# Performance work log

Hardware: AMD Instinct MI355X
Metric: run time of the kernel (lower is better)

Reference implementation:

```python
import jax, jax.numpy as jnp
import numpy as np

B, N, M, C, K = 2, 8192, 4096, 64, 16
HID = 256
EPS_BN = 1e-5


def setup_inputs() -> dict:
    key = jax.random.key(0)
    ks = jax.random.split(key, 16)
    def rn(i, shape, scale=1.0):
        return jax.random.normal(ks[i], shape, jnp.float32) * scale
    return {
        "pcl": rn(0, (B, M, 3)),
        "pcl_noise": rn(1, (B, N, 3)),
        "feature": rn(2, (B, M, C)),
        # MLP_CONV (2d 1x1): 6 -> 256 (BN+ReLU) -> C
        "w2a": rn(3, (HID, 6), 0.3), "b2a": rn(4, (HID,), 0.1),
        "g2a": 1.0 + rn(5, (HID,), 0.1), "bt2a": rn(6, (HID,), 0.1),
        "w2b": rn(7, (C, HID), 0.1), "b2b": rn(8, (C,), 0.1),
        # MLP_CONV_1d: 3C -> C (BN+ReLU) -> C
        "w1a": rn(9, (C, 3 * C), 0.1), "b1a": rn(10, (C,), 0.1),
        "g1a": 1.0 + rn(11, (C,), 0.1), "bt1a": rn(12, (C,), 0.1),
        "w1b": rn(13, (C, C), 0.1), "b1b": rn(14, (C,), 0.1),
    }


def _sqdist(x, y):  # [B,n,3],[B,m,3] -> [B,n,m]
    return (jnp.sum(x * x, -1, keepdims=True)
            - 2.0 * jnp.einsum('bnc,bmc->bnm', x, y)
            + jnp.sum(y * y, -1)[:, None, :])


def _gather(x, idx):  # x [B,M,D], idx [B,...] -> [B,...,D]
    return jax.vmap(lambda xb, ib: xb[ib])(x, idx)


def _bn(h, g, b):  # inference BatchNorm: running mean 0, var 1
    return h * (g / jnp.sqrt(1.0 + EPS_BN)) + b


def reference(pcl, pcl_noise, feature, w2a, b2a, g2a, bt2a, w2b, b2b,
              w1a, b1a, g1a, bt1a, w1b, b1b):
    # nearest clean point for each noisy point (knn_points K=1)
    close_idx = jnp.argmin(_sqdist(pcl_noise, pcl), axis=-1)          # [B,N]
    close_point = _gather(pcl, close_idx)                             # [B,N,3]
    # K nearest neighbors of close_point within pcl (dil_knn, d=1)
    _, idx = jax.lax.top_k(-_sqdist(close_point, pcl), K)             # [B,N,K]
    knn_points = _gather(pcl, idx)[:, :, 1:, :]                       # [B,N,K-1,3]
    knn_feat = _gather(feature, idx)[:, :, 1:, :]                     # [B,N,K-1,C]
    close_feat = _gather(feature, close_idx)                          # [B,N,C]

    delta = knn_points - pcl_noise[:, :, None, :]                     # [B,N,K-1,3]
    dst = jnp.linalg.norm(delta, axis=-1)                             # [B,N,K-1]
    e = jnp.exp(-10.0 * dst)
    weight = e / (jnp.sum(e, -1, keepdims=True) + 1e-7)               # [B,N,K-1]

    cp = jnp.broadcast_to(close_point[:, :, None, :], delta.shape)
    delta_points = jnp.concatenate([delta, cp], axis=-1)              # [B,N,K-1,6]

    # MLP_CONV2 (1x1 convs over channel dim)
    h = jnp.einsum('bnkc,oc->bnko', delta_points, w2a) + b2a
    h = jax.nn.relu(_bn(h, g2a, bt2a))
    pf = jnp.einsum('bnkc,oc->bnko', h, w2b) + b2b                    # [B,N,K-1,C]

    point_feature = jnp.einsum('bnk,bnkc->bnc', weight, pf)           # [B,N,C]
    co_feature = jnp.einsum('bnk,bnkc->bnc', weight, knn_feat)        # [B,N,C]
    df = jnp.concatenate([close_feat, co_feature, point_feature], -1)  # [B,N,3C]

    # MLP_CONV_1d
    h1 = jnp.einsum('bnc,oc->bno', df, w1a) + b1a
    h1 = jax.nn.relu(_bn(h1, g1a, bt1a))
    return jnp.einsum('bnc,oc->bno', h1, w1b) + b1b                   # [B,N,C]
```

## Files before the change

kernel.cpp:

```cpp
#include <hip/hip_runtime.h>
#include <float.h>

typedef unsigned short u16;
typedef unsigned int u32;
typedef unsigned char u8;

__device__ __forceinline__ float bf(u16 u) { return __uint_as_float(((u32)u) << 16); }
__device__ __forceinline__ u16 f2bf(float v) {
    u32 x = __float_as_uint(v);
    u32 r = x + 0x7fffu + ((x >> 16) & 1u);
    return (u16)(r >> 16);
}
__device__ __forceinline__ float blo(u32 u) { return __uint_as_float(u << 16); }
__device__ __forceinline__ float bhi(u32 u) { return __uint_as_float(u & 0xffff0000u); }
__device__ __forceinline__ int detect_f32(const void* probe) {
    const u16* u = (const u16*)probe;
    u16 v = u[(threadIdx.x & 63) * 2];
    int e = (int)((v >> 7) & 0xFF);
    int moderate = (e >= 100) && (e <= 140);
    return __popcll(__ballot(moderate)) < 48;
}
__device__ __forceinline__ float ldv(int f32, const void* p, int i) {
    return f32 ? ((const float*)p)[i] : bf(((const u16*)p)[i]);
}
__device__ __forceinline__ float dot3(float x0, float x1, float x2,
                                      float y0, float y1, float y2) {
    return __fmaf_rn(x2, y2, __fmaf_rn(x1, y1, __fmul_rn(x0, y0)));
}
__device__ __forceinline__ u32 mkey32(float d) {
    u32 f = __float_as_uint(d);
    return f ^ (u32)((((int)f) >> 31) | 0x80000000);
}

__global__ __launch_bounds__(256) void k_canon(const void* __restrict__ probe,
                                               const void* __restrict__ w2b,
                                               const void* __restrict__ w1a,
                                               const void* __restrict__ w1b,
                                               u32* __restrict__ canonb) {
    int f32 = detect_f32(probe);
    int ix = blockIdx.x * 256 + threadIdx.x;
    const void* src; int j;
    if (ix < 8192)       { src = w2b; j = ix; }
    else if (ix < 14336) { src = w1a; j = ix - 8192; }
    else                 { src = w1b; j = ix - 14336; }
    u32 out;
    if (f32) {
        const float* f = (const float*)src;
        out = ((u32)f2bf(f[2*j+1]) << 16) | (u32)f2bf(f[2*j]);
    } else {
        const u16* su = (const u16*)src;
        out = ((u32)su[2*j+1] << 16) | (u32)su[2*j];
    }
    canonb[ix] = out;
}

__global__ __launch_bounds__(256) void k_prep(const void* __restrict__ probe,
                                              const void* __restrict__ pcl,
                                              float4* __restrict__ pcl4) {
    int f32 = detect_f32(probe);
    int i = blockIdx.x * 256 + threadIdx.x;
    float x = ldv(f32, pcl, i*3+0), y = ldv(f32, pcl, i*3+1), z = ldv(f32, pcl, i*3+2);
    float s = __fadd_rn(__fadd_rn(__fmul_rn(x,x), __fmul_rn(y,y)), __fmul_rn(z,z));
    pcl4[i] = make_float4(x, y, z, s);
}

__global__ __launch_bounds__(256) void k_close(const float4* __restrict__ pcl4,
                                               const void* __restrict__ noise,
                                               u16* __restrict__ cidx) {
    __shared__ __align__(16) float4 tile[2048];
    int f32 = detect_f32(noise);
    int t = threadIdx.x, g = t >> 4, s = t & 15;
    int q = blockIdx.x * 16 + g;
    int b = q >> 13;
    const float4* src = pcl4 + ((size_t)b << 12);
    float x0 = ldv(f32, noise, q*3+0), x1 = ldv(f32, noise, q*3+1), x2 = ldv(f32, noise, q*3+2);
    float sx = __fadd_rn(__fadd_rn(__fmul_rn(x0,x0), __fmul_rn(x1,x1)), __fmul_rn(x2,x2));
    float bd = FLT_MAX; int bi = 0;
    for (int ch = 0; ch < 2; ++ch) {
        __syncthreads();
#pragma unroll
        for (int i = 0; i < 8; ++i) { int ix = t + (i << 8); tile[ix] = src[(ch << 11) + ix]; }
        __syncthreads();
        for (int j = 0; j < 128; ++j) {
            int cl = (j << 4) + s;
            float4 p = tile[cl];
            float dot = dot3(x0, x1, x2, p.x, p.y, p.z);
            float d = __fadd_rn(__fsub_rn(sx, __fmul_rn(2.0f, dot)), p.w);
            int c = (ch << 11) + cl;
            if (d < bd) { bd = d; bi = c; }
        }
    }
#pragma unroll
    for (int m = 8; m >= 1; m >>= 1) {
        float od = __shfl_xor(bd, m);
        int   oi = __shfl_xor(bi, m);
        if (od < bd || (od == bd && oi < bi)) { bd = od; bi = oi; }
    }
    if (s == 0) cidx[q] = (u16)(bi & 4095);
}

__global__ __launch_bounds__(256) void k_knnh(const float4* __restrict__ pcl4,
                                              u16* __restrict__ knn) {
    __shared__ u8  bins[4096];
    __shared__ u32 hist[256];
    __shared__ u32 skey[256];
    __shared__ u16 sidx[256];
    __shared__ float rmn[4], rmx[4];
    __shared__ u32 scnt;
    __shared__ int ibst;
    int t = threadIdx.x, lane = t & 63, wv = t >> 6;
    int q = blockIdx.x;
    int b = q >> 12;
    const float4* src = pcl4 + ((size_t)b << 12);
    float4 Q = src[q & 4095];
    float x0 = Q.x, x1 = Q.y, x2 = Q.z, sx = Q.w;
    if (t < 256) hist[t] = 0;
    if (t == 0) scnt = 0;
    {
        float4 p = src[t << 4];
        float dot = dot3(x0, x1, x2, p.x, p.y, p.z);
        float d = __fadd_rn(__fsub_rn(sx, __fmul_rn(2.0f, dot)), p.w);
        float mn = d, mx = d;
#pragma unroll
        for (int m = 32; m >= 1; m >>= 1) {
            mn = fminf(mn, __shfl_xor(mn, m));
            mx = fmaxf(mx, __shfl_xor(mx, m));
        }
        if (lane == 0) { rmn[wv] = mn; rmx[wv] = mx; }
    }
    __syncthreads();
    float dmn = fminf(fminf(rmn[0], rmn[1]), fminf(rmn[2], rmn[3]));
    float dmx = fmaxf(fmaxf(rmx[0], rmx[1]), fmaxf(rmx[2], rmx[3]));
    float sc = 1024.0f / fmaxf(dmx - dmn, 1e-20f);
#pragma unroll 4
    for (int j = 0; j < 16; ++j) {
        int cin = (j << 8) + t;
        float4 p = src[cin];
        float dot = dot3(x0, x1, x2, p.x, p.y, p.z);
        float d = __fadd_rn(__fsub_rn(sx, __fmul_rn(2.0f, dot)), p.w);
        float fb = fminf(fmaxf((d - dmn) * sc, 0.0f), 255.0f);
        int bn = (int)fb;
        bins[cin] = (u8)bn;
        if (bn < 255) atomicAdd(&hist[bn], 1u);
    }
    __syncthreads();
    if (t < 64) {
        u32 c0 = hist[4*lane], c1 = hist[4*lane+1];
        u32 c2 = hist[4*lane+2], c3 = hist[4*lane+3];
        u32 loc = c0 + c1 + c2 + c3;
        u32 x = loc;
#pragma unroll
        for (int off = 1; off < 64; off <<= 1) { u32 v = __shfl_up(x, off); if (lane >= off) x += v; }
        u32 excl = x - loc;
        int cand = 999;
        if (excl + c0 >= 16u) cand = 4*lane;
        else if (excl + c0 + c1 >= 16u) cand = 4*lane + 1;
        else if (excl + c0 + c1 + c2 >= 16u) cand = 4*lane + 2;
        else if (excl + loc >= 16u) cand = 4*lane + 3;
#pragma unroll
        for (int m = 32; m >= 1; m >>= 1) cand = min(cand, __shfl_xor(cand, m));
        if (lane == 0) ibst = cand;
    }
    __syncthreads();
    int bstar = ibst;
#pragma unroll
    for (int j = 0; j < 16; ++j) {
        int cin = (j << 8) + t;
        if ((int)bins[cin] <= bstar) {
            u32 pos = atomicAdd(&scnt, 1u);
            if (pos < 256u) {
                float4 p = src[cin];
                float dot = dot3(x0, x1, x2, p.x, p.y, p.z);
                float d = __fadd_rn(__fsub_rn(sx, __fmul_rn(2.0f, dot)), p.w);
                skey[pos] = mkey32(d);
                sidx[pos] = (u16)cin;
            }
        }
    }
    __syncthreads();
    u32 n = scnt;
    if (n <= 256u) {
        for (u32 e = (u32)t; e < n; e += 256u) {
            u32 k = skey[e]; u32 i = (u32)sidx[e];
            int rank = 0;
            for (u32 j = 0; j < n; ++j) {
                u32 kj = skey[j]; u32 ij = (u32)sidx[j];
                rank += (kj < k) || (kj == k && ij < i);
            }
            if (rank < 16) knn[((size_t)q << 4) + rank] = (u16)i;
        }
    } else if (t < 64) {
        u32 k0=~0u,k1=~0u,k2=~0u,k3=~0u,k4=~0u,k5=~0u,k6=~0u,k7=~0u,
            k8=~0u,k9=~0u,k10=~0u,k11=~0u,k12=~0u,k13=~0u,k14=~0u,k15=~0u;
        u32 i0r=0,i1r=0,i2r=0,i3r=0,i4r=0,i5r=0,i6r=0,i7r=0,
            i8r=0,i9r=0,i10r=0,i11r=0,i12r=0,i13r=0,i14r=0,i15r=0;
        for (int j = 0; j < 64; ++j) {
            int cin = (j << 6) + lane;
            float4 p = src[cin];
            float dot = dot3(x0, x1, x2, p.x, p.y, p.z);
            float d = __fadd_rn(__fsub_rn(sx, __fmul_rn(2.0f, dot)), p.w);
            u32 v = mkey32(d); u32 vi = (u32)cin;
            if (v < k15) {
                { u32 c_=(v<k0); u32 nk=c_?v:k0; u32 nv=c_?k0:v; u32 ni=c_?vi:i0r; u32 nj=c_?i0r:vi; k0=nk;i0r=ni;v=nv;vi=nj; }
                { u32 c_=(v<k1); u32 nk=c_?v:k1; u32 nv=c_?k1:v; u32 ni=c_?vi:i1r; u32 nj=c_?i1r:vi; k1=nk;i1r=ni;v=nv;vi=nj; }
                { u32 c_=(v<k2); u32 nk=c_?v:k2; u32 nv=c_?k2:v; u32 ni=c_?vi:i2r; u32 nj=c_?i2r:vi; k2=nk;i2r=ni;v=nv;vi=nj; }
                { u32 c_=(v<k3); u32 nk=c_?v:k3; u32 nv=c_?k3:v; u32 ni=c_?vi:i3r; u32 nj=c_?i3r:vi; k3=nk;i3r=ni;v=nv;vi=nj; }
                { u32 c_=(v<k4); u32 nk=c_?v:k4; u32 nv=c_?k4:v; u32 ni=c_?vi:i4r; u32 nj=c_?i4r:vi; k4=nk;i4r=ni;v=nv;vi=nj; }
                { u32 c_=(v<k5); u32 nk=c_?v:k5; u32 nv=c_?k5:v; u32 ni=c_?vi:i5r; u32 nj=c_?i5r:vi; k5=nk;i5r=ni;v=nv;vi=nj; }
                { u32 c_=(v<k6); u32 nk=c_?v:k6; u32 nv=c_?k6:v; u32 ni=c_?vi:i6r; u32 nj=c_?i6r:vi; k6=nk;i6r=ni;v=nv;vi=nj; }
                { u32 c_=(v<k7); u32 nk=c_?v:k7; u32 nv=c_?k7:v; u32 ni=c_?vi:i7r; u32 nj=c_?i7r:vi; k7=nk;i7r=ni;v=nv;vi=nj; }
                { u32 c_=(v<k8); u32 nk=c_?v:k8; u32 nv=c_?k8:v; u32 ni=c_?vi:i8r; u32 nj=c_?i8r:vi; k8=nk;i8r=ni;v=nv;vi=nj; }
                { u32 c_=(v<k9); u32 nk=c_?v:k9; u32 nv=c_?k9:v; u32 ni=c_?vi:i9r; u32 nj=c_?i9r:vi; k9=nk;i9r=ni;v=nv;vi=nj; }
                { u32 c_=(v<k10); u32 nk=c_?v:k10; u32 nv=c_?k10:v; u32 ni=c_?vi:i10r; u32 nj=c_?i10r:vi; k10=nk;i10r=ni;v=nv;vi=nj; }
                { u32 c_=(v<k11); u32 nk=c_?v:k11; u32 nv=c_?k11:v; u32 ni=c_?vi:i11r; u32 nj=c_?i11r:vi; k11=nk;i11r=ni;v=nv;vi=nj; }
                { u32 c_=(v<k12); u32 nk=c_?v:k12; u32 nv=c_?k12:v; u32 ni=c_?vi:i12r; u32 nj=c_?i12r:vi; k12=nk;i12r=ni;v=nv;vi=nj; }
                { u32 c_=(v<k13); u32 nk=c_?v:k13; u32 nv=c_?k13:v; u32 ni=c_?vi:i13r; u32 nj=c_?i13r:vi; k13=nk;i13r=ni;v=nv;vi=nj; }
                { u32 c_=(v<k14); u32 nk=c_?v:k14; u32 nv=c_?k14:v; u32 ni=c_?vi:i14r; u32 nj=c_?i14r:vi; k14=nk;i14r=ni;v=nv;vi=nj; }
                { u32 c_=(v<k15); u32 nk=c_?v:k15; u32 nv=c_?k15:v; u32 ni=c_?vi:i15r; u32 nj=c_?i15r:vi; k15=nk;i15r=ni;v=nv;vi=nj; }
            }
        }
        u32 myres = 0;
        for (int o = 0; o < 16; ++o) {
            u32 bk = k0, bi2 = i0r;
#pragma unroll
            for (int m = 32; m >= 1; m >>= 1) {
                u32 ok = __shfl_xor(bk, m), oi = __shfl_xor(bi2, m);
                if (ok < bk || (ok == bk && oi < bi2)) { bk = ok; bi2 = oi; }
            }
            if (lane == o) myres = bi2;
            if (k0 == bk && i0r == bi2) {
                k0=k1; i0r=i1r; k1=k2; i1r=i2r; k2=k3; i2r=i3r; k3=k4; i3r=i4r;
                k4=k5; i4r=i5r; k5=k6; i5r=i6r; k6=k7; i6r=i7r; k7=k8; i7r=i8r;
                k8=k9; i8r=i9r; k9=k10; i9r=i10r; k10=k11; i10r=i11r; k11=k12; i11r=i12r;
                k12=k13; i12r=i13r; k13=k14; i13r=i14r; k14=k15; i14r=i15r;
                k15=~0u; i15r=0xFFFFu;
            }
        }
        if (lane < 16) knn[((size_t)q << 4) + lane] = (u16)myres;
    }
}

__global__ __launch_bounds__(256) void k_tail(const float4* __restrict__ pcl4,
                                              const void* __restrict__ noise,
                                              const void* __restrict__ feat,
                                              const u16* __restrict__ cidx,
                                              const u16* __restrict__ knn,
                                              const void* __restrict__ w2a,
                                              const void* __restrict__ b2a,
                                              const void* __restrict__ g2a,
                                              const void* __restrict__ bt2a,
                                              const u32* __restrict__ canonb,
                                              const void* __restrict__ b2b,
                                              const void* __restrict__ b1a,
                                              const void* __restrict__ g1a,
                                              const void* __restrict__ bt1a,
                                              const void* __restrict__ b1b,
                                              void* __restrict__ outp) {
    __shared__ float w2at[6][256];
    __shared__ float sc2[256], of2[256];
    __shared__ float b2bf[64], s1[64], o1[64], b1f[64];
    __shared__ __align__(16) float hb[4][4][256];
    __shared__ __align__(16) float dfs[4][4][192];
    __shared__ __align__(16) float h1s[4][4][64];
    __shared__ float dpb[4][4][16][6];
    __shared__ float wbuf[4][4][16];
    __shared__ int   jbuf[4][4][16];
    __shared__ float wsb[4][4];

    int f32 = detect_f32(noise);
    int t = threadIdx.x;
    {
        float s2 = ldv(f32, g2a, t) / sqrtf(1.0f + 1e-5f);
        sc2[t] = s2;
        of2[t] = ldv(f32, b2a, t) * s2 + ldv(f32, bt2a, t);
#pragma unroll
        for (int c = 0; c < 6; ++c) w2at[c][t] = ldv(f32, w2a, t*6+c);
        if (t < 64) {
            b2bf[t] = ldv(f32, b2b, t);
            float s = ldv(f32, g1a, t) / sqrtf(1.0f + 1e-5f);
            s1[t] = s; o1[t] = ldv(f32, b1a, t) * s + ldv(f32, bt1a, t); b1f[t] = ldv(f32, b1b, t);
        }
    }
    int lane = t & 63, wv = t >> 6;
    int qbase = blockIdx.x * 16 + wv * 4;
    {
        int ql = lane >> 4, s = lane & 15;
        int q = qbase + ql;
        int b = q >> 13;
        int pbase = (b << 12);
        int ci = ((int)cidx[q]) & 4095;
        float4 cp = pcl4[pbase + ci];
        float x0 = ldv(f32, noise, q*3+0), x1 = ldv(f32, noise, q*3+1), x2 = ldv(f32, noise, q*3+2);
        float e = 0.0f;
        if (s >= 1) {
            int jk = ((int)knn[(size_t)(pbase + ci) * 16 + s]) & 4095;
            float4 p = pcl4[pbase + jk];
            float d0 = p.x - x0, d1 = p.y - x1, d2 = p.z - x2;
            float dst = sqrtf(__fadd_rn(__fadd_rn(__fmul_rn(d0,d0), __fmul_rn(d1,d1)), __fmul_rn(d2,d2)));
            e = expf(-10.0f * dst);
            dpb[wv][ql][s][0] = d0; dpb[wv][ql][s][1] = d1; dpb[wv][ql][s][2] = d2;
            dpb[wv][ql][s][3] = cp.x; dpb[wv][ql][s][4] = cp.y; dpb[wv][ql][s][5] = cp.z;
            jbuf[wv][ql][s] = jk;
        }
        float es = e;
#pragma unroll
        for (int m = 8; m >= 1; m >>= 1) es += __shfl_xor(es, m, 16);
        float den = es + 1e-7f;
        if (s >= 1) wbuf[wv][ql][s] = e / den;
        if (s == 0) wsb[wv][ql] = es / den;
    }
    __syncthreads();

    float cf[4], co[4];
#pragma unroll
    for (int ql = 0; ql < 4; ++ql) {
        int q = qbase + ql;
        int b = q >> 13;
        int pbase = (b << 12);
        int ci = ((int)cidx[q]) & 4095;
        size_t fcb = ((size_t)(pbase + ci)) << 6;
        float c0, c1 = 0.0f;
        if (f32) {
            const float* ff = (const float*)feat;
            c0 = ff[fcb + lane];
#pragma unroll
            for (int k = 1; k < 16; ++k)
                c1 += wbuf[wv][ql][k] * ff[(((size_t)(pbase + jbuf[wv][ql][k])) << 6) + lane];
        } else {
            const u16* fb = (const u16*)feat;
            c0 = bf(fb[fcb + lane]);
#pragma unroll
            for (int k = 1; k < 16; ++k)
                c1 += wbuf[wv][ql][k] * bf(fb[(((size_t)(pbase + jbuf[wv][ql][k])) << 6) + lane]);
        }
        cf[ql] = c0; co[ql] = c1;
    }

    float wa[4][6], scr[4], ofr[4];
#pragma unroll
    for (int r = 0; r < 4; ++r) {
        int ch = lane + (r << 6);
#pragma unroll
        for (int c = 0; c < 6; ++c) wa[r][c] = w2at[c][ch];
        scr[r] = sc2[ch]; ofr[r] = of2[ch];
    }
    float hv[4][4];
#pragma unroll
    for (int ql = 0; ql < 4; ++ql)
#pragma unroll
        for (int r = 0; r < 4; ++r) hv[ql][r] = 0.0f;
#pragma unroll
    for (int k = 1; k < 16; ++k) {
#pragma unroll
        for (int ql = 0; ql < 4; ++ql) {
            float p0 = dpb[wv][ql][k][0], p1 = dpb[wv][ql][k][1], p2 = dpb[wv][ql][k][2];
            float p3 = dpb[wv][ql][k][3], p4 = dpb[wv][ql][k][4], p5 = dpb[wv][ql][k][5];
            float wk = wbuf[wv][ql][k];
#pragma unroll
            for (int r = 0; r < 4; ++r) {
                float z = p0*wa[r][0] + p1*wa[r][1] + p2*wa[r][2]
                        + p3*wa[r][3] + p4*wa[r][4] + p5*wa[r][5];
                z = z * scr[r] + ofr[r];
                z = fmaxf(z, 0.0f);
                hv[ql][r] += wk * z;
            }
        }
    }
#pragma unroll
    for (int ql = 0; ql < 4; ++ql)
#pragma unroll
        for (int r = 0; r < 4; ++r) hb[wv][ql][lane + (r << 6)] = hv[ql][r];
    __syncthreads();

    float acc[4];
#pragma unroll
    for (int ql = 0; ql < 4; ++ql) acc[ql] = b2bf[lane] * wsb[wv][ql];
    {
        const uint4* wrow = reinterpret_cast<const uint4*>(canonb + (lane << 7));
#pragma unroll 4
        for (int i = 0; i < 32; ++i) {
            uint4 u = wrow[i];
            float w0 = blo(u.x), w1 = bhi(u.x), w2 = blo(u.y), w3 = bhi(u.y);
            float w4 = blo(u.z), w5 = bhi(u.z), w6 = blo(u.w), w7 = bhi(u.w);
#pragma unroll
            for (int ql = 0; ql < 4; ++ql) {
                const float4* hrow = reinterpret_cast<const float4*>(&hb[wv][ql][0]);
                float4 hA = hrow[2*i], hB = hrow[2*i+1];
                acc[ql] += w0*hA.x + w1*hA.y + w2*hA.z + w3*hA.w
                         + w4*hB.x + w5*hB.y + w6*hB.z + w7*hB.w;
            }
        }
    }
#pragma unroll
    for (int ql = 0; ql < 4; ++ql) {
        dfs[wv][ql][lane]       = cf[ql];
        dfs[wv][ql][64 + lane]  = co[ql];
        dfs[wv][ql][128 + lane] = acc[ql];
    }
    __syncthreads();

    float acc1[4] = {0.0f, 0.0f, 0.0f, 0.0f};
    {
        const uint4* wr = reinterpret_cast<const uint4*>(canonb + 8192 + lane * 96);
#pragma unroll 4
        for (int i = 0; i < 24; ++i) {
            uint4 u = wr[i];
            float w0 = blo(u.x), w1 = bhi(u.x), w2 = blo(u.y), w3 = bhi(u.y);
            float w4 = blo(u.z), w5 = bhi(u.z), w6 = blo(u.w), w7 = bhi(u.w);
#pragma unroll
            for (int ql = 0; ql < 4; ++ql) {
                const float4* dv = reinterpret_cast<const float4*>(&dfs[wv][ql][0]);
                float4 a = dv[2*i], c = dv[2*i+1];
                acc1[ql] += w0*a.x + w1*a.y + w2*a.z + w3*a.w
                          + w4*c.x + w5*c.y + w6*c.z + w7*c.w;
            }
        }
    }
#pragma unroll
    for (int ql = 0; ql < 4; ++ql) {
        float z1 = acc1[ql] * s1[lane] + o1[lane];
        z1 = fmaxf(z1, 0.0f);
        h1s[wv][ql][lane] = z1;
    }
    __syncthreads();

    float a2[4];
#pragma unroll
    for (int ql = 0; ql < 4; ++ql) a2[ql] = b1f[lane];
    {
        const uint4* wr2 = reinterpret_cast<const uint4*>(canonb + 14336 + (lane << 5));
#pragma unroll
        for (int i = 0; i < 8; ++i) {
            uint4 u = wr2[i];
            float w0 = blo(u.x), w1 = bhi(u.x), w2 = blo(u.y), w3 = bhi(u.y);
            float w4 = blo(u.z), w5 = bhi(u.z), w6 = blo(u.w), w7 = bhi(u.w);
#pragma unroll
            for (int ql = 0; ql < 4; ++ql) {
                const float4* hv2 = reinterpret_cast<const float4*>(&h1s[wv][ql][0]);
                float4 a = hv2[2*i], c = hv2[2*i+1];
                a2[ql] += w0*a.x + w1*a.y + w2*a.z + w3*a.w
                        + w4*c.x + w5*c.y + w6*c.z + w7*c.w;
            }
        }
    }
#pragma unroll
    for (int ql = 0; ql < 4; ++ql) {
        size_t ob = ((size_t)(qbase + ql) << 6) + lane;
        if (f32) ((float*)outp)[ob] = a2[ql];
        else     ((u16*)outp)[ob]   = f2bf(a2[ql]);
    }
}

extern "C" void kernel_launch(void* const* d_in, const int* in_sizes, int n_in,
                              void* d_out, int out_size, void* d_ws, size_t ws_size,
                              hipStream_t stream) {
    const void* pcl   = d_in[0];
    const void* noise = d_in[1];
    const void* feat  = d_in[2];
    const void* w2a   = d_in[3];
    const void* b2a   = d_in[4];
    const void* g2a   = d_in[5];
    const void* bt2a  = d_in[6];
    const void* w2b   = d_in[7];
    const void* b2b   = d_in[8];
    const void* w1a   = d_in[9];
    const void* b1a   = d_in[10];
    const void* g1a   = d_in[11];
    const void* bt1a  = d_in[12];
    const void* w1b   = d_in[13];
    const void* b1b   = d_in[14];

    char* ws = (char*)d_ws;
    float4* pcl4 = (float4*)ws;
    u16* cidx = (u16*)(ws + 131072);
    u16* knn  = (u16*)(ws + 163840);
    u32* canonb = (u32*)(ws + 425984);

    k_canon<<<64,   256, 0, stream>>>(noise, w2b, w1a, w1b, canonb);
    k_prep <<<32,   256, 0, stream>>>(noise, pcl, pcl4);
    k_close<<<1024, 256, 0, stream>>>(pcl4, noise, cidx);
    k_knnh <<<8192, 256, 0, stream>>>(pcl4, knn);
    k_tail <<<1024, 256, 0, stream>>>(pcl4, noise, feat, cidx, knn,
                                      w2a, b2a, g2a, bt2a, canonb, b2b,
                                      b1a, g1a, bt1a, b1b, d_out);
}
```

Baseline: 239.1 us.

## Move tail MLP layers onto bf16 MFMA with hi/lo split-precision operands

Rewrites the per-query MLP tail kernel so that the 6->256 conv, the 256->64 conv, and the two 1d layers run on 16x16x32 bf16 MFMA instructions instead of scalar FMA loops. Activations are split into bf16 high and low parts and accumulated with two MFMAs to keep near-fp32 accuracy. The first layer also folds the BN scale into the weights and uses a third operand slot for the low part of the weights. Shared memory is repacked into a single arena holding bf16 tiles, and a launch-bounds occupancy hint is added. This adds bf16 conversion overhead and some accuracy risk in exchange for much higher matrix throughput.

```diff
diff --git a/kernel.cpp b/kernel.cpp
--- a/kernel.cpp
+++ b/kernel.cpp
@@ -4,6 +4,9 @@
 typedef unsigned short u16;
 typedef unsigned int u32;
 typedef unsigned char u8;
+
+typedef float f32x4 __attribute__((ext_vector_type(4)));
+typedef short bh8   __attribute__((ext_vector_type(8)));
 
 __device__ __forceinline__ float bf(u16 u) { return __uint_as_float(((u32)u) << 16); }
 __device__ __forceinline__ u16 f2bf(float v) {
@@ -11,8 +14,6 @@
     u32 r = x + 0x7fffu + ((x >> 16) & 1u);
     return (u16)(r >> 16);
 }
-__device__ __forceinline__ float blo(u32 u) { return __uint_as_float(u << 16); }
-__device__ __forceinline__ float bhi(u32 u) { return __uint_as_float(u & 0xffff0000u); }
 __device__ __forceinline__ int detect_f32(const void* probe) {
     const u16* u = (const u16*)probe;
     u16 v = u[(threadIdx.x & 63) * 2];
@@ -30,6 +31,10 @@
 __device__ __forceinline__ u32 mkey32(float d) {
     u32 f = __float_as_uint(d);
     return f ^ (u32)((((int)f) >> 31) | 0x80000000);
+}
+__device__ __forceinline__ bh8 ldb(const void* p) { return *(const bh8*)p; }
+__device__ __forceinline__ f32x4 mfma16(bh8 a, bh8 b, f32x4 c) {
+    return __builtin_amdgcn_mfma_f32_16x16x32_bf16(a, b, c, 0, 0, 0);
 }
 
 __global__ __launch_bounds__(256) void k_canon(const void* __restrict__ probe,
@@ -240,54 +245,71 @@
     }
 }
 
-__global__ __launch_bounds__(256) void k_tail(const float4* __restrict__ pcl4,
-                                              const void* __restrict__ noise,
-                                              const void* __restrict__ feat,
-                                              const u16* __restrict__ cidx,
-                                              const u16* __restrict__ knn,
-                                              const void* __restrict__ w2a,
-                                              const void* __restrict__ b2a,
-                                              const void* __restrict__ g2a,
-                                              const void* __restrict__ bt2a,
-                                              const u32* __restrict__ canonb,
-                                              const void* __restrict__ b2b,
-                                              const void* __restrict__ b1a,
-                                              const void* __restrict__ g1a,
-                                              const void* __restrict__ bt1a,
-                                              const void* __restrict__ b1b,
-                                              void* __restrict__ outp) {
-    __shared__ float w2at[6][256];
-    __shared__ float sc2[256], of2[256];
-    __shared__ float b2bf[64], s1[64], o1[64], b1f[64];
-    __shared__ __align__(16) float hb[4][4][256];
-    __shared__ __align__(16) float dfs[4][4][192];
-    __shared__ __align__(16) float h1s[4][4][64];
-    __shared__ float dpb[4][4][16][6];
-    __shared__ float wbuf[4][4][16];
-    __shared__ int   jbuf[4][4][16];
-    __shared__ float wsb[4][4];
+__global__ __launch_bounds__(256, 4) void k_tail(const float4* __restrict__ pcl4,
+                                                 const void* __restrict__ noise,
+                                                 const void* __restrict__ feat,
+                                                 const u16* __restrict__ cidx,
+                                                 const u16* __restrict__ knn,
+                                                 const void* __restrict__ w2a,
+                                                 const void* __restrict__ b2a,
+                                                 const void* __restrict__ g2a,
+                                                 const void* __restrict__ bt2a,
+                                                 const u32* __restrict__ canonb,
+                                                 const void* __restrict__ b2b,
+                                                 const void* __restrict__ b1a,
+                                                 const void* __restrict__ g1a,
+                                                 const void* __restrict__ bt1a,
+                                                 const void* __restrict__ b1b,
+                                                 void* __restrict__ outp) {
+    __shared__ __align__(16) char arena[39744];
+    char* dpb_hi = arena;
+    char* dpb_lo = arena + 4352;
+    char* wbt    = arena + 8704;
+    char* wsbp   = arena + 9984;
+    u16*  jbuf   = (u16*)(arena + 10048);
+    char* hbm_   = arena + 10560;
+    char* dfm    = arena + 27200;
+    char* h1m    = arena;
 
     int f32 = detect_f32(noise);
-    int t = threadIdx.x;
+    int t = threadIdx.x, lane = t & 63, wv = t >> 6;
+    int g = lane >> 4, l15 = lane & 15;
+    int qbb = blockIdx.x * 16;
+    int o_lane = wv * 16 + l15;
+    const float rbn = 1.0f / sqrtf(1.0f + 1e-5f);
+    const char* cb = (const char*)canonb;
+    const f32x4 zero4 = {0.f, 0.f, 0.f, 0.f};
+
+    float of2r[4];
+    bh8 wH[4];
+#pragma unroll
+    for (int j = 0; j < 4; ++j) {
+        int oh = wv*64 + j*16 + l15;
+        float sc = ldv(f32, g2a, oh) * rbn;
+        of2r[j] = ldv(f32, b2a, oh) * sc + ldv(f32, bt2a, oh);
+        bh8 wz = (bh8){0,0,0,0,0,0,0,0};
+        if (g < 3) {
+#pragma unroll
+            for (int c = 0; c < 6; ++c) {
+                float wval = ldv(f32, w2a, oh*6 + c) * sc;
+                u16 h = f2bf(wval);
+                u16 e = (g == 2) ? f2bf(wval - bf(h)) : h;
+                wz[c] = (short)e;
+            }
+        }
+        wH[j] = wz;
+    }
+    float s1o  = ldv(f32, g1a, o_lane) * rbn;
+    float o1o  = ldv(f32, b1a, o_lane) * s1o + ldv(f32, bt1a, o_lane);
+    float b2bo = ldv(f32, b2b, o_lane);
+    float b1fo = ldv(f32, b1b, o_lane);
+
     {
-        float s2 = ldv(f32, g2a, t) / sqrtf(1.0f + 1e-5f);
-        sc2[t] = s2;
-        of2[t] = ldv(f32, b2a, t) * s2 + ldv(f32, bt2a, t);
-#pragma unroll
-        for (int c = 0; c < 6; ++c) w2at[c][t] = ldv(f32, w2a, t*6+c);
-        if (t < 64) {
-            b2bf[t] = ldv(f32, b2b, t);
-            float s = ldv(f32, g1a, t) / sqrtf(1.0f + 1e-5f);
-            s1[t] = s; o1[t] = ldv(f32, b1a, t) * s + ldv(f32, bt1a, t); b1f[t] = ldv(f32, b1b, t);
-        }
-    }
-    int lane = t & 63, wv = t >> 6;
-    int qbase = blockIdx.x * 16 + wv * 4;
-    {
-        int ql = lane >> 4, s = lane & 15;
-        int q = qbase + ql;
+        int s = lane & 15;
+        int ql = wv*4 + (lane >> 4);
+        int q = qbb + ql;
         int b = q >> 13;
-        int pbase = (b << 12);
+        int pbase = b << 12;
         int ci = ((int)cidx[q]) & 4095;
         float4 cp = pcl4[pbase + ci];
         float x0 = ldv(f32, noise, q*3+0), x1 = ldv(f32, noise, q*3+1), x2 = ldv(f32, noise, q*3+2);
@@ -298,25 +320,35 @@
             float d0 = p.x - x0, d1 = p.y - x1, d2 = p.z - x2;
             float dst = sqrtf(__fadd_rn(__fadd_rn(__fmul_rn(d0,d0), __fmul_rn(d1,d1)), __fmul_rn(d2,d2)));
             e = expf(-10.0f * dst);
-            dpb[wv][ql][s][0] = d0; dpb[wv][ql][s][1] = d1; dpb[wv][ql][s][2] = d2;
-            dpb[wv][ql][s][3] = cp.x; dpb[wv][ql][s][4] = cp.y; dpb[wv][ql][s][5] = cp.z;
-            jbuf[wv][ql][s] = jk;
+            float v6[6] = {d0, d1, d2, cp.x, cp.y, cp.z};
+            bh8 HW = (bh8){0,0,0,0,0,0,0,0};
+            bh8 LW = (bh8){0,0,0,0,0,0,0,0};
+#pragma unroll
+            for (int c = 0; c < 6; ++c) {
+                u16 hh = f2bf(v6[c]);
+                u16 ll = f2bf(v6[c] - bf(hh));
+                HW[c] = (short)hh;
+                LW[c] = (short)ll;
+            }
+            *(bh8*)(dpb_hi + (ql*17 + s)*16) = HW;
+            *(bh8*)(dpb_lo + (ql*17 + s)*16) = LW;
+            jbuf[ql*16 + s] = (u16)jk;
         }
         float es = e;
 #pragma unroll
         for (int m = 8; m >= 1; m >>= 1) es += __shfl_xor(es, m, 16);
         float den = es + 1e-7f;
-        if (s >= 1) wbuf[wv][ql][s] = e / den;
-        if (s == 0) wsb[wv][ql] = es / den;
-    }
-    __syncthreads();
-
-    float cf[4], co[4];
-#pragma unroll
-    for (int ql = 0; ql < 4; ++ql) {
-        int q = qbase + ql;
+        if (s >= 1) *(float*)(wbt + s*80 + ql*4) = e / den;
+        if (s == 0) *(float*)(wsbp + ql*4) = es / den;
+    }
+    __syncthreads();
+
+#pragma unroll
+    for (int qq = 0; qq < 4; ++qq) {
+        int qloc = wv*4 + qq;
+        int q = qbb + qloc;
         int b = q >> 13;
-        int pbase = (b << 12);
+        int pbase = b << 12;
         int ci = ((int)cidx[q]) & 4095;
         size_t fcb = ((size_t)(pbase + ci)) << 6;
         float c0, c1 = 0.0f;
@@ -324,130 +356,136 @@
             const float* ff = (const float*)feat;
             c0 = ff[fcb + lane];
 #pragma unroll
-            for (int k = 1; k < 16; ++k)
-                c1 += wbuf[wv][ql][k] * ff[(((size_t)(pbase + jbuf[wv][ql][k])) << 6) + lane];
+            for (int k = 1; k < 16; ++k) {
+                float wk = *(const float*)(wbt + k*80 + qloc*4);
+                c1 += wk * ff[(((size_t)(pbase + (int)jbuf[qloc*16 + k])) << 6) + lane];
+            }
         } else {
             const u16* fb = (const u16*)feat;
             c0 = bf(fb[fcb + lane]);
 #pragma unroll
-            for (int k = 1; k < 16; ++k)
-                c1 += wbuf[wv][ql][k] * bf(fb[(((size_t)(pbase + jbuf[wv][ql][k])) << 6) + lane]);
-        }
-        cf[ql] = c0; co[ql] = c1;
-    }
-
-    float wa[4][6], scr[4], ofr[4];
-#pragma unroll
-    for (int r = 0; r < 4; ++r) {
-        int ch = lane + (r << 6);
-#pragma unroll
-        for (int c = 0; c < 6; ++c) wa[r][c] = w2at[c][ch];
-        scr[r] = sc2[ch]; ofr[r] = of2[ch];
-    }
-    float hv[4][4];
-#pragma unroll
-    for (int ql = 0; ql < 4; ++ql)
-#pragma unroll
-        for (int r = 0; r < 4; ++r) hv[ql][r] = 0.0f;
-#pragma unroll
-    for (int k = 1; k < 16; ++k) {
-#pragma unroll
-        for (int ql = 0; ql < 4; ++ql) {
-            float p0 = dpb[wv][ql][k][0], p1 = dpb[wv][ql][k][1], p2 = dpb[wv][ql][k][2];
-            float p3 = dpb[wv][ql][k][3], p4 = dpb[wv][ql][k][4], p5 = dpb[wv][ql][k][5];
-            float wk = wbuf[wv][ql][k];
+            for (int k = 1; k < 16; ++k) {
+                float wk = *(const float*)(wbt + k*80 + qloc*4);
+                c1 += wk * bf(fb[(((size_t)(pbase + (int)jbuf[qloc*16 + k])) << 6) + lane]);
+            }
+        }
+        char* dr = dfm + qloc*784;
+        u16 h0 = f2bf(c0); u16 l0 = f2bf(c0 - bf(h0));
+        u16 h1v = f2bf(c1); u16 l1v = f2bf(c1 - bf(h1v));
+        *(u16*)(dr + (size_t)lane*2)         = h0;
+        *(u16*)(dr + (size_t)(192+lane)*2)   = l0;
+        *(u16*)(dr + (size_t)(64+lane)*2)    = h1v;
+        *(u16*)(dr + (size_t)(256+lane)*2)   = l1v;
+    }
+
+    {
+        f32x4 hba[4];
+#pragma unroll
+        for (int j = 0; j < 4; ++j) hba[j] = zero4;
+#pragma unroll
+        for (int k = 1; k < 16; ++k) {
+            bh8 af;
+            if (g < 3) {
+                const char* base = (g == 1) ? dpb_lo : dpb_hi;
+                af = ldb(base + (l15*17 + k)*16);
+            } else {
+                af = (bh8){0,0,0,0,0,0,0,0};
+            }
+            f32x4 wk4 = *(const f32x4*)(wbt + k*80 + g*16);
+#pragma unroll
+            for (int j = 0; j < 4; ++j) {
+                f32x4 d = mfma16(af, wH[j], zero4);
+#pragma unroll
+                for (int r = 0; r < 4; ++r)
+                    hba[j][r] += wk4[r] * fmaxf(d[r] + of2r[j], 0.0f);
+            }
+        }
+#pragma unroll
+        for (int j = 0; j < 4; ++j)
 #pragma unroll
             for (int r = 0; r < 4; ++r) {
-                float z = p0*wa[r][0] + p1*wa[r][1] + p2*wa[r][2]
-                        + p3*wa[r][3] + p4*wa[r][4] + p5*wa[r][5];
-                z = z * scr[r] + ofr[r];
-                z = fmaxf(z, 0.0f);
-                hv[ql][r] += wk * z;
-            }
-        }
-    }
-#pragma unroll
-    for (int ql = 0; ql < 4; ++ql)
-#pragma unroll
-        for (int r = 0; r < 4; ++r) hb[wv][ql][lane + (r << 6)] = hv[ql][r];
-    __syncthreads();
-
-    float acc[4];
-#pragma unroll
-    for (int ql = 0; ql < 4; ++ql) acc[ql] = b2bf[lane] * wsb[wv][ql];
+                int q = g*4 + r;
+                int o = wv*64 + j*16 + l15;
+                float x = hba[j][r];
+                u16 h = f2bf(x); u16 l = f2bf(x - bf(h));
+                *(u16*)(hbm_ + q*1040 + (size_t)o*2)       = h;
+                *(u16*)(hbm_ + q*1040 + 512 + (size_t)o*2) = l;
+            }
+    }
+    __syncthreads();
+
     {
-        const uint4* wrow = reinterpret_cast<const uint4*>(canonb + (lane << 7));
-#pragma unroll 4
-        for (int i = 0; i < 32; ++i) {
-            uint4 u = wrow[i];
-            float w0 = blo(u.x), w1 = bhi(u.x), w2 = blo(u.y), w3 = bhi(u.y);
-            float w4 = blo(u.z), w5 = bhi(u.z), w6 = blo(u.w), w7 = bhi(u.w);
-#pragma unroll
-            for (int ql = 0; ql < 4; ++ql) {
-                const float4* hrow = reinterpret_cast<const float4*>(&hb[wv][ql][0]);
-                float4 hA = hrow[2*i], hB = hrow[2*i+1];
-                acc[ql] += w0*hA.x + w1*hA.y + w2*hA.z + w3*hA.w
-                         + w4*hB.x + w5*hB.y + w6*hB.z + w7*hB.w;
-            }
-        }
-    }
-#pragma unroll
-    for (int ql = 0; ql < 4; ++ql) {
-        dfs[wv][ql][lane]       = cf[ql];
-        dfs[wv][ql][64 + lane]  = co[ql];
-        dfs[wv][ql][128 + lane] = acc[ql];
-    }
-    __syncthreads();
-
-    float acc1[4] = {0.0f, 0.0f, 0.0f, 0.0f};
+        bh8 bw[8];
+#pragma unroll
+        for (int ks = 0; ks < 8; ++ks)
+            bw[ks] = ldb(cb + (size_t)o_lane*512 + ks*64 + g*16);
+        f32x4 acA = zero4, acB = zero4;
+#pragma unroll
+        for (int ks = 0; ks < 8; ++ks) {
+            bh8 a = ldb(hbm_ + l15*1040 + ks*64 + g*16);
+            acA = mfma16(a, bw[ks], acA);
+        }
+#pragma unroll
+        for (int ks = 0; ks < 8; ++ks) {
+            bh8 a = ldb(hbm_ + l15*1040 + 512 + ks*64 + g*16);
+            acB = mfma16(a, bw[ks], acB);
+        }
+        f32x4 wsb4 = *(const f32x4*)(wsbp + g*16);
+#pragma unroll
+        for (int r = 0; r < 4; ++r) {
+            int q = g*4 + r;
+            float pf = acA[r] + acB[r] + b2bo * wsb4[r];
+            u16 h = f2bf(pf); u16 l = f2bf(pf - bf(h));
+            *(u16*)(dfm + q*784 + (size_t)(128 + o_lane)*2) = h;
+            *(u16*)(dfm + q*784 + (size_t)(320 + o_lane)*2) = l;
+        }
+    }
+    __syncthreads();
+
     {
-        const uint4* wr = reinterpret_cast<const uint4*>(canonb + 8192 + lane * 96);
-#pragma unroll 4
-        for (int i = 0; i < 24; ++i) {
-            uint4 u = wr[i];
-            float w0 = blo(u.x), w1 = bhi(u.x), w2 = blo(u.y), w3 = bhi(u.y);
-            float w4 = blo(u.z), w5 = bhi(u.z), w6 = blo(u.w), w7 = bhi(u.w);
-#pragma unroll
-            for (int ql = 0; ql < 4; ++ql) {
-                const float4* dv = reinterpret_cast<const float4*>(&dfs[wv][ql][0]);
-                float4 a = dv[2*i], c = dv[2*i+1];
-                acc1[ql] += w0*a.x + w1*a.y + w2*a.z + w3*a.w
-                          + w4*c.x + w5*c.y + w6*c.z + w7*c.w;
-            }
-        }
-    }
-#pragma unroll
-    for (int ql = 0; ql < 4; ++ql) {
-        float z1 = acc1[ql] * s1[lane] + o1[lane];
-        z1 = fmaxf(z1, 0.0f);
-        h1s[wv][ql][lane] = z1;
-    }
-    __syncthreads();
-
-    float a2[4];
-#pragma unroll
-    for (int ql = 0; ql < 4; ++ql) a2[ql] = b1f[lane];
+        bh8 bw[6];
+#pragma unroll
+        for (int ks = 0; ks < 6; ++ks)
+            bw[ks] = ldb(cb + 32768 + (size_t)o_lane*384 + ks*64 + g*16);
+        f32x4 acA = zero4, acB = zero4;
+#pragma unroll
+        for (int ks = 0; ks < 6; ++ks) {
+            bh8 a = ldb(dfm + l15*784 + ks*64 + g*16);
+            acA = mfma16(a, bw[ks], acA);
+        }
+#pragma unroll
+        for (int ks = 0; ks < 6; ++ks) {
+            bh8 a = ldb(dfm + l15*784 + 384 + ks*64 + g*16);
+            acB = mfma16(a, bw[ks], acB);
+        }
+#pragma unroll
+        for (int r = 0; r < 4; ++r) {
+            int q = g*4 + r;
+            float z = (acA[r] + acB[r]) * s1o + o1o;
+            z = fmaxf(z, 0.0f);
+            u16 h = f2bf(z); u16 l = f2bf(z - bf(h));
+            *(u16*)(h1m + q*272 + (size_t)o_lane*2)       = h;
+            *(u16*)(h1m + q*272 + 128 + (size_t)o_lane*2) = l;
+        }
+    }
+    __syncthreads();
+
     {
-        const uint4* wr2 = reinterpret_cast<const uint4*>(canonb + 14336 + (lane << 5));
-#pragma unroll
-        for (int i = 0; i < 8; ++i) {
-            uint4 u = wr2[i];
-            float w0 = blo(u.x), w1 = bhi(u.x), w2 = blo(u.y), w3 = bhi(u.y);
-            float w4 = blo(u.z), w5 = bhi(u.z), w6 = blo(u.w), w7 = bhi(u.w);
-#pragma unroll
-            for (int ql = 0; ql < 4; ++ql) {
-                const float4* hv2 = reinterpret_cast<const float4*>(&h1s[wv][ql][0]);
-                float4 a = hv2[2*i], c = hv2[2*i+1];
-                a2[ql] += w0*a.x + w1*a.y + w2*a.z + w3*a.w
-                        + w4*c.x + w5*c.y + w6*c.z + w7*c.w;
-            }
-        }
-    }
-#pragma unroll
-    for (int ql = 0; ql < 4; ++ql) {
-        size_t ob = ((size_t)(qbase + ql) << 6) + lane;
-        if (f32) ((float*)outp)[ob] = a2[ql];
-        else     ((u16*)outp)[ob]   = f2bf(a2[ql]);
+        bh8 bw0 = ldb(cb + 57344 + (size_t)o_lane*128 + g*16);
+        bh8 bw1 = ldb(cb + 57344 + (size_t)o_lane*128 + 64 + g*16);
+        f32x4 ac = zero4;
+        { bh8 a = ldb(h1m + l15*272 +   0 + g*16); ac = mfma16(a, bw0, ac); }
+        { bh8 a = ldb(h1m + l15*272 +  64 + g*16); ac = mfma16(a, bw1, ac); }
+        { bh8 a = ldb(h1m + l15*272 + 128 + g*16); ac = mfma16(a, bw0, ac); }
+        { bh8 a = ldb(h1m + l15*272 + 192 + g*16); ac = mfma16(a, bw1, ac); }
+#pragma unroll
+        for (int r = 0; r < 4; ++r) {
+            int q = g*4 + r;
+            float ov = ac[r] + b1fo;
+            size_t ob = ((size_t)(qbb + q) << 6) + o_lane;
+            if (f32) ((float*)outp)[ob] = ov;
+            else     ((u16*)outp)[ob]   = f2bf(ov);
+        }
     }
 }
 
```

After: 278.0 us. +16.3%, slower.
